# Kernel optimization log

Hardware: AMD Instinct MI355X
Metric: run time of the kernel (lower is better)

## Reference

```python
import jax, jax.numpy as jnp
import numpy as np

V, H, E, L = 50257, 1024, 1024, 512


def setup_inputs() -> dict:
    key = jax.random.key(0)
    ks = jax.random.split(key, 16)
    s = 0.02  # init scale
    return {
        "input_token": jax.random.randint(ks[0], (1,), 0, V),
        "hidden": jax.random.normal(ks[1], (1, 1, H), jnp.float32),
        "encoder_outputs": jax.random.normal(ks[2], (L, H), jnp.float32),
        "embedding": jax.random.normal(ks[3], (V, E), jnp.float32) * s,
        "attn_w": jax.random.normal(ks[4], (L, H + E), jnp.float32) * s,
        "attn_b": jnp.zeros((L,), jnp.float32),
        "comb_w": jax.random.normal(ks[5], (E, H + E), jnp.float32) * s,
        "comb_b": jnp.zeros((E,), jnp.float32),
        "w_ih": jax.random.normal(ks[6], (3 * H, E), jnp.float32) * s,
        "w_hh": jax.random.normal(ks[7], (3 * H, H), jnp.float32) * s,
        "b_ih": jnp.zeros((3 * H,), jnp.float32),
        "b_hh": jnp.zeros((3 * H,), jnp.float32),
        "out_w": jax.random.normal(ks[8], (V, H), jnp.float32) * s,
        "out_b": jnp.zeros((V,), jnp.float32),
    }


def reference(input_token, hidden, encoder_outputs, embedding, attn_w, attn_b,
              comb_w, comb_b, w_ih, w_hh, b_ih, b_hh, out_w, out_b):
    # embedded = embedding(input).view(1,1,-1); dropout is identity in eval
    emb = embedding[input_token].reshape(1, E)            # [1, E]
    h0 = hidden[0]                                        # [1, H]
    # attention over encoder positions
    attn_logits = jnp.concatenate([emb, h0], axis=1) @ attn_w.T + attn_b  # [1, L]
    attn_weights = jax.nn.softmax(attn_logits, axis=1)
    attn_applied = attn_weights @ encoder_outputs         # [1, H]
    # combine + relu
    x = jnp.concatenate([emb, attn_applied], axis=1) @ comb_w.T + comb_b  # [1, E]
    x = jax.nn.relu(x)
    # single GRU cell step (PyTorch gate order: r, z, n)
    gi = x @ w_ih.T + b_ih                                # [1, 3H]
    gh = h0 @ w_hh.T + b_hh                               # [1, 3H]
    i_r, i_z, i_n = jnp.split(gi, 3, axis=1)
    h_r, h_z, h_n = jnp.split(gh, 3, axis=1)
    r = jax.nn.sigmoid(i_r + h_r)
    z = jax.nn.sigmoid(i_z + h_z)
    n = jnp.tanh(i_n + r * h_n)
    h_new = (1.0 - z) * n + z * h0                        # [1, H]
    # output projection + log softmax
    logits = h_new @ out_w.T + out_b                      # [1, V]
    out = jax.nn.log_softmax(logits, axis=1)
    return out, h_new[None], attn_weights
```

## Files before the change

kernel.cpp:

```cpp
#include <hip/hip_runtime.h>

#define V 50257
#define H 1024
#define E 1024
#define LENC 512

__device__ __forceinline__ float wave_reduce_sum(float v) {
    #pragma unroll
    for (int off = 32; off > 0; off >>= 1)
        v += __shfl_down(v, off, 64);
    return v;
}

__global__ void dotcat_kernel(const float* __restrict__ W,
                              const float* __restrict__ bias,
                              const float* __restrict__ emb_table,
                              const int*   __restrict__ token,
                              const float* __restrict__ b,
                              float* __restrict__ out,
                              int relu) {
    int wid = threadIdx.x >> 6, lane = threadIdx.x & 63;
    int row = blockIdx.x * 4 + wid;
    const float4* w4 = (const float4*)(W + (size_t)row * 2048);
    const float4* e4 = (const float4*)(emb_table + (size_t)(*token) * 1024);
    const float4* b4 = (const float4*)b;
    float acc = 0.f;
    #pragma unroll
    for (int j = 0; j < 4; ++j) {
        float4 w = w4[lane + 64 * j];
        float4 x = e4[lane + 64 * j];
        acc += w.x * x.x + w.y * x.y + w.z * x.z + w.w * x.w;
    }
    #pragma unroll
    for (int j = 0; j < 4; ++j) {
        float4 w = w4[256 + lane + 64 * j];
        float4 x = b4[lane + 64 * j];
        acc += w.x * x.x + w.y * x.y + w.z * x.z + w.w * x.w;
    }
    acc = wave_reduce_sum(acc);
    if (lane == 0) {
        acc += bias[row];
        if (relu) acc = fmaxf(acc, 0.0f);
        out[row] = acc;
    }
}

__global__ void softmax512_kernel(const float* __restrict__ in,
                                  float* __restrict__ out,
                                  float* __restrict__ aapp) {
    int t = threadIdx.x;
    aapp[t] = 0.f;
    aapp[512 + t] = 0.f;
    float x = in[t];
    float m = x;
    #pragma unroll
    for (int off = 32; off > 0; off >>= 1)
        m = fmaxf(m, __shfl_down(m, off, 64));
    __shared__ float sm[8];
    __shared__ float ss[8];
    int lane = t & 63, wid = t >> 6;
    if (lane == 0) sm[wid] = m;
    __syncthreads();
    if (t == 0) {
        float mm = sm[0];
        #pragma unroll
        for (int i = 1; i < 8; ++i) mm = fmaxf(mm, sm[i]);
        sm[0] = mm;
    }
    __syncthreads();
    float M = sm[0];
    float e = expf(x - M);
    float s = e;
    #pragma unroll
    for (int off = 32; off > 0; off >>= 1)
        s += __shfl_down(s, off, 64);
    if (lane == 0) ss[wid] = s;
    __syncthreads();
    if (t == 0) {
        float tot = 0.f;
        #pragma unroll
        for (int i = 0; i < 8; ++i) tot += ss[i];
        ss[0] = tot;
    }
    __syncthreads();
    out[t] = e / ss[0];
}

__global__ void attn_apply_kernel(const float* __restrict__ weights,
                                  const float* __restrict__ enc,
                                  float* __restrict__ aapp) {
    int h  = blockIdx.x * 256 + threadIdx.x;
    int l0 = blockIdx.y * 32;
    float acc = 0.f;
    #pragma unroll 8
    for (int l = 0; l < 32; ++l)
        acc += weights[l0 + l] * enc[(size_t)(l0 + l) * 1024 + h];
    atomicAdd(&aapp[h], acc);
}

__global__ void gru_fused_kernel(const float* __restrict__ w_ih,
                                 const float* __restrict__ w_hh,
                                 const float* __restrict__ b_ih,
                                 const float* __restrict__ b_hh,
                                 const float* __restrict__ x,
                                 const float* __restrict__ h0,
                                 float* __restrict__ hnew) {
    int j = blockIdx.x;
    int g = threadIdx.x >> 6, lane = threadIdx.x & 63;
    int sel = g / 3;
    int gate = g % 3;
    int row = gate * 1024 + j;
    const float* Wm  = sel ? w_hh : w_ih;
    const float* vin = sel ? h0 : x;
    const float* bia = sel ? b_hh : b_ih;
    const float4* w4 = (const float4*)(Wm + (size_t)row * 1024);
    const float4* v4 = (const float4*)vin;
    float acc = 0.f;
    #pragma unroll
    for (int jj = 0; jj < 4; ++jj) {
        float4 w = w4[lane + 64 * jj];
        float4 v = v4[lane + 64 * jj];
        acc += w.x * v.x + w.y * v.y + w.z * v.z + w.w * v.w;
    }
    acc = wave_reduce_sum(acc);
    __shared__ float s[6];
    if (lane == 0) s[g] = acc + bia[row];
    __syncthreads();
    if (threadIdx.x == 0) {
        float r = 1.0f / (1.0f + expf(-(s[0] + s[3])));
        float z = 1.0f / (1.0f + expf(-(s[1] + s[4])));
        float n = tanhf(s[2] + r * s[5]);
        hnew[j] = (1.0f - z) * n + z * h0[j];
    }
}

__global__ void logits_kernel(const float* __restrict__ out_w,
                              const float* __restrict__ out_b,
                              const float* __restrict__ h,
                              float* __restrict__ logits,
                              float* __restrict__ part) {
    int wid = threadIdx.x >> 6, lane = threadIdx.x & 63;
    int gw = blockIdx.x * 4 + wid;
    const float4* h4 = (const float4*)h;
    float4 x0 = h4[lane], x1 = h4[lane + 64], x2 = h4[lane + 128], x3 = h4[lane + 192];
    float psum = 0.f;
    for (int row = gw; row < V; row += 8192) {
        const float4* w4 = (const float4*)(out_w + (size_t)row * 1024);
        float4 w0 = w4[lane], w1 = w4[lane + 64], w2 = w4[lane + 128], w3 = w4[lane + 192];
        float acc = w0.x * x0.x + w0.y * x0.y + w0.z * x0.z + w0.w * x0.w
                  + w1.x * x1.x + w1.y * x1.y + w1.z * x1.z + w1.w * x1.w
                  + w2.x * x2.x + w2.y * x2.y + w2.z * x2.z + w2.w * x2.w
                  + w3.x * x3.x + w3.y * x3.y + w3.z * x3.z + w3.w * x3.w;
        acc = wave_reduce_sum(acc);
        if (lane == 0) {
            acc += out_b[row];
            logits[row] = acc;
            psum += expf(acc);
        }
    }
    __shared__ float s[4];
    if (lane == 0) s[wid] = psum;
    __syncthreads();
    if (threadIdx.x == 0) part[blockIdx.x] = s[0] + s[1] + s[2] + s[3];
}

__global__ void logsub_kernel(float* __restrict__ out,
                              const float* __restrict__ part) {
    float v = 0.f;
    #pragma unroll
    for (int i = threadIdx.x; i < 2048; i += 256) v += part[i];
    v = wave_reduce_sum(v);
    __shared__ float s[4];
    int lane = threadIdx.x & 63, wid = threadIdx.x >> 6;
    if (lane == 0) s[wid] = v;
    __syncthreads();
    float lse = logf(s[0] + s[1] + s[2] + s[3]);
    int i = blockIdx.x * 256 + threadIdx.x;
    if (i < V) out[i] -= lse;
}

extern "C" void kernel_launch(void* const* d_in, const int* in_sizes, int n_in,
                              void* d_out, int out_size, void* d_ws, size_t ws_size,
                              hipStream_t stream) {
    const int*   token     = (const int*)d_in[0];
    const float* hidden    = (const float*)d_in[1];
    const float* enc       = (const float*)d_in[2];
    const float* emb_table = (const float*)d_in[3];
    const float* attn_w    = (const float*)d_in[4];
    const float* attn_b    = (const float*)d_in[5];
    const float* comb_w    = (const float*)d_in[6];
    const float* comb_b    = (const float*)d_in[7];
    const float* w_ih      = (const float*)d_in[8];
    const float* w_hh      = (const float*)d_in[9];
    const float* b_ih      = (const float*)d_in[10];
    const float* b_hh      = (const float*)d_in[11];
    const float* out_w     = (const float*)d_in[12];
    const float* out_b     = (const float*)d_in[13];

    float* out       = (float*)d_out;
    float* hnew_out  = out + V;
    float* attnw_out = out + V + H;

    float* wsf  = (float*)d_ws;
    float* alog = wsf;
    float* aapp = alog + 512;
    float* xbuf = aapp + 1024;
    float* part = xbuf + 1024;

    dotcat_kernel<<<LENC / 4, 256, 0, stream>>>(attn_w, attn_b, emb_table, token,
                                                hidden, alog, 0);
    softmax512_kernel<<<1, 512, 0, stream>>>(alog, attnw_out, aapp);
    attn_apply_kernel<<<dim3(4, 16), 256, 0, stream>>>(attnw_out, enc, aapp);
    dotcat_kernel<<<E / 4, 256, 0, stream>>>(comb_w, comb_b, emb_table, token,
                                             aapp, xbuf, 1);
    gru_fused_kernel<<<H, 384, 0, stream>>>(w_ih, w_hh, b_ih, b_hh, xbuf, hidden,
                                            hnew_out);
    logits_kernel<<<2048, 256, 0, stream>>>(out_w, out_b, hnew_out, out, part);
    logsub_kernel<<<(V + 255) / 256, 256, 0, stream>>>(out, part);
}
```

Before: 57.96 us.

## Restructure decoder stages and prefetch output weights into cache during dependent chain

```diff
diff --git a/kernel.cpp b/kernel.cpp
--- a/kernel.cpp
+++ b/kernel.cpp
@@ -4,6 +4,8 @@
 #define H 1024
 #define E 1024
 #define LENC 512
+#define GBLK 1024
+#define GWAVES (GBLK * 4)
 
 __device__ __forceinline__ float wave_reduce_sum(float v) {
     #pragma unroll
@@ -12,18 +14,125 @@
     return v;
 }
 
-__global__ void dotcat_kernel(const float* __restrict__ W,
-                              const float* __restrict__ bias,
+__device__ __forceinline__ void prefetch_chunk(const float* __restrict__ out_w,
+                                               int chunk) {
+    const float4* p = (const float4*)out_w + (size_t)chunk * 4096;
+    float acc = 0.f;
+    #pragma unroll 4
+    for (int i = threadIdx.x; i < 4096; i += 256) {
+        float4 v = p[i];
+        acc += v.x + v.y + v.z + v.w;
+    }
+    asm volatile("" ::"v"(acc));
+}
+
+__global__ void stageA_kernel(const float* __restrict__ attn_w,
+                              const float* __restrict__ attn_b,
+                              const float* __restrict__ w_hh,
+                              const float* __restrict__ b_hh,
                               const float* __restrict__ emb_table,
                               const int*   __restrict__ token,
-                              const float* __restrict__ b,
-                              float* __restrict__ out,
-                              int relu) {
+                              const float* __restrict__ hidden,
+                              const float* __restrict__ out_w,
+                              float* __restrict__ alog,
+                              float* __restrict__ g,
+                              float* __restrict__ aapp) {
+    int bx = blockIdx.x;
     int wid = threadIdx.x >> 6, lane = threadIdx.x & 63;
-    int row = blockIdx.x * 4 + wid;
-    const float4* w4 = (const float4*)(W + (size_t)row * 2048);
+    if (bx < 128) {
+        int row = bx * 4 + wid;
+        const float4* w4 = (const float4*)(attn_w + (size_t)row * 2048);
+        const float4* e4 = (const float4*)(emb_table + (size_t)(*token) * 1024);
+        const float4* h4 = (const float4*)hidden;
+        float acc = 0.f;
+        #pragma unroll
+        for (int j = 0; j < 4; ++j) {
+            float4 w = w4[lane + 64 * j];
+            float4 x = e4[lane + 64 * j];
+            acc += w.x * x.x + w.y * x.y + w.z * x.z + w.w * x.w;
+        }
+        #pragma unroll
+        for (int j = 0; j < 4; ++j) {
+            float4 w = w4[256 + lane + 64 * j];
+            float4 x = h4[lane + 64 * j];
+            acc += w.x * x.x + w.y * x.y + w.z * x.z + w.w * x.w;
+        }
+        acc = wave_reduce_sum(acc);
+        if (lane == 0) alog[row] = acc + attn_b[row];
+    } else if (bx < 896) {
+        int row = (bx - 128) * 4 + wid;
+        const float4* w4 = (const float4*)(w_hh + (size_t)row * 1024);
+        const float4* h4 = (const float4*)hidden;
+        float acc = 0.f;
+        #pragma unroll
+        for (int j = 0; j < 4; ++j) {
+            float4 w = w4[lane + 64 * j];
+            float4 x = h4[lane + 64 * j];
+            acc += w.x * x.x + w.y * x.y + w.z * x.z + w.w * x.w;
+        }
+        acc = wave_reduce_sum(acc);
+        if (lane == 0) g[3072 + row] = acc + b_hh[row];
+    } else if (bx == 896) {
+        int t = threadIdx.x;
+        aapp[t] = 0.f; aapp[256 + t] = 0.f; aapp[512 + t] = 0.f; aapp[768 + t] = 0.f;
+    } else {
+        prefetch_chunk(out_w, bx - 897);
+    }
+}
+
+__global__ void stageC_kernel(const float* __restrict__ alog,
+                              const float* __restrict__ enc,
+                              const float* __restrict__ out_w,
+                              float* __restrict__ aapp,
+                              float* __restrict__ attnw_out) {
+    int bx = blockIdx.x;
+    if (bx >= 256) { prefetch_chunk(out_w, 160 + bx - 256); return; }
+    int t = threadIdx.x;
+    int lane = t & 63, wid = t >> 6;
+    __shared__ float eb[512];
+    __shared__ float sm[4], ssum[4];
+    float a0 = alog[t], a1 = alog[t + 256];
+    float m = fmaxf(a0, a1);
+    #pragma unroll
+    for (int off = 32; off > 0; off >>= 1)
+        m = fmaxf(m, __shfl_down(m, off, 64));
+    if (lane == 0) sm[wid] = m;
+    __syncthreads();
+    float M = fmaxf(fmaxf(sm[0], sm[1]), fmaxf(sm[2], sm[3]));
+    float e0 = expf(a0 - M), e1 = expf(a1 - M);
+    eb[t] = e0; eb[t + 256] = e1;
+    float s = e0 + e1;
+    s = wave_reduce_sum(s);
+    if (lane == 0) ssum[wid] = s;
+    __syncthreads();
+    float S = ssum[0] + ssum[1] + ssum[2] + ssum[3];
+    if (bx == 0) {
+        attnw_out[t] = eb[t] / S;
+        attnw_out[t + 256] = eb[t + 256] / S;
+    }
+    int h  = (bx & 3) * 256 + t;
+    int l0 = (bx >> 2) * 8;
+    float acc = 0.f;
+    #pragma unroll
+    for (int l = 0; l < 8; ++l)
+        acc += eb[l0 + l] * enc[(size_t)(l0 + l) * 1024 + h];
+    atomicAdd(&aapp[h], acc / S);
+}
+
+__global__ void stageD_kernel(const float* __restrict__ comb_w,
+                              const float* __restrict__ comb_b,
+                              const float* __restrict__ emb_table,
+                              const int*   __restrict__ token,
+                              const float* __restrict__ aapp,
+                              const float* __restrict__ out_w,
+                              float* __restrict__ xbuf) {
+    int bx = blockIdx.x;
+    if (bx >= 256) { prefetch_chunk(out_w, 320 + bx - 256); return; }
+    int wid = threadIdx.x >> 6, lane = threadIdx.x & 63;
+    int row = bx * 4 + wid;
+    const float4* w4 = (const float4*)(comb_w + (size_t)row * 2048);
     const float4* e4 = (const float4*)(emb_table + (size_t)(*token) * 1024);
-    const float4* b4 = (const float4*)b;
+    const float4* a4 = (const float4*)aapp;
     float acc = 0.f;
     #pragma unroll
     for (int j = 0; j < 4; ++j) {
@@ -34,117 +143,61 @@
     #pragma unroll
     for (int j = 0; j < 4; ++j) {
         float4 w = w4[256 + lane + 64 * j];
-        float4 x = b4[lane + 64 * j];
+        float4 x = a4[lane + 64 * j];
         acc += w.x * x.x + w.y * x.y + w.z * x.z + w.w * x.w;
     }
     acc = wave_reduce_sum(acc);
-    if (lane == 0) {
-        acc += bias[row];
-        if (relu) acc = fmaxf(acc, 0.0f);
-        out[row] = acc;
-    }
-}
-
-__global__ void softmax512_kernel(const float* __restrict__ in,
-                                  float* __restrict__ out,
-                                  float* __restrict__ aapp) {
+    if (lane == 0) xbuf[row] = fmaxf(acc + comb_b[row], 0.0f);
+}
+
+__global__ void stageE_kernel(const float* __restrict__ w_ih,
+                              const float* __restrict__ b_ih,
+                              const float* __restrict__ xbuf,
+                              const float* __restrict__ out_w,
+                              float* __restrict__ g) {
+    int bx = blockIdx.x;
+    if (bx >= 768) { prefetch_chunk(out_w, 480 + bx - 768); return; }
+    int wid = threadIdx.x >> 6, lane = threadIdx.x & 63;
+    int row = bx * 4 + wid;
+    const float4* w4 = (const float4*)(w_ih + (size_t)row * 1024);
+    const float4* x4 = (const float4*)xbuf;
+    float acc = 0.f;
+    #pragma unroll
+    for (int j = 0; j < 4; ++j) {
+        float4 w = w4[lane + 64 * j];
+        float4 x = x4[lane + 64 * j];
+        acc += w.x * x.x + w.y * x.y + w.z * x.z + w.w * x.w;
+    }
+    acc = wave_reduce_sum(acc);
+    if (lane == 0) g[row] = acc + b_ih[row];
+}
+
+__global__ void logits_kernel(const float* __restrict__ g,
+                              const float* __restrict__ hidden,
+                              const float* __restrict__ out_w,
+                              const float* __restrict__ out_b,
+                              float* __restrict__ logits,
+                              float* __restrict__ part,
+                              float* __restrict__ hnew_out) {
+    __shared__ float4 hsm4[256];
+    float* hs = (float*)hsm4;
     int t = threadIdx.x;
-    aapp[t] = 0.f;
-    aapp[512 + t] = 0.f;
-    float x = in[t];
-    float m = x;
-    #pragma unroll
-    for (int off = 32; off > 0; off >>= 1)
-        m = fmaxf(m, __shfl_down(m, off, 64));
-    __shared__ float sm[8];
-    __shared__ float ss[8];
-    int lane = t & 63, wid = t >> 6;
-    if (lane == 0) sm[wid] = m;
-    __syncthreads();
-    if (t == 0) {
-        float mm = sm[0];
-        #pragma unroll
-        for (int i = 1; i < 8; ++i) mm = fmaxf(mm, sm[i]);
-        sm[0] = mm;
-    }
-    __syncthreads();
-    float M = sm[0];
-    float e = expf(x - M);
-    float s = e;
-    #pragma unroll
-    for (int off = 32; off > 0; off >>= 1)
-        s += __shfl_down(s, off, 64);
-    if (lane == 0) ss[wid] = s;
-    __syncthreads();
-    if (t == 0) {
-        float tot = 0.f;
-        #pragma unroll
-        for (int i = 0; i < 8; ++i) tot += ss[i];
-        ss[0] = tot;
-    }
-    __syncthreads();
-    out[t] = e / ss[0];
-}
-
-__global__ void attn_apply_kernel(const float* __restrict__ weights,
-                                  const float* __restrict__ enc,
-                                  float* __restrict__ aapp) {
-    int h  = blockIdx.x * 256 + threadIdx.x;
-    int l0 = blockIdx.y * 32;
-    float acc = 0.f;
-    #pragma unroll 8
-    for (int l = 0; l < 32; ++l)
-        acc += weights[l0 + l] * enc[(size_t)(l0 + l) * 1024 + h];
-    atomicAdd(&aapp[h], acc);
-}
-
-__global__ void gru_fused_kernel(const float* __restrict__ w_ih,
-                                 const float* __restrict__ w_hh,
-                                 const float* __restrict__ b_ih,
-                                 const float* __restrict__ b_hh,
-                                 const float* __restrict__ x,
-                                 const float* __restrict__ h0,
-                                 float* __restrict__ hnew) {
-    int j = blockIdx.x;
-    int g = threadIdx.x >> 6, lane = threadIdx.x & 63;
-    int sel = g / 3;
-    int gate = g % 3;
-    int row = gate * 1024 + j;
-    const float* Wm  = sel ? w_hh : w_ih;
-    const float* vin = sel ? h0 : x;
-    const float* bia = sel ? b_hh : b_ih;
-    const float4* w4 = (const float4*)(Wm + (size_t)row * 1024);
-    const float4* v4 = (const float4*)vin;
-    float acc = 0.f;
-    #pragma unroll
-    for (int jj = 0; jj < 4; ++jj) {
-        float4 w = w4[lane + 64 * jj];
-        float4 v = v4[lane + 64 * jj];
-        acc += w.x * v.x + w.y * v.y + w.z * v.z + w.w * v.w;
-    }
-    acc = wave_reduce_sum(acc);
-    __shared__ float s[6];
-    if (lane == 0) s[g] = acc + bia[row];
-    __syncthreads();
-    if (threadIdx.x == 0) {
-        float r = 1.0f / (1.0f + expf(-(s[0] + s[3])));
-        float z = 1.0f / (1.0f + expf(-(s[1] + s[4])));
-        float n = tanhf(s[2] + r * s[5]);
-        hnew[j] = (1.0f - z) * n + z * h0[j];
-    }
-}
-
-__global__ void logits_kernel(const float* __restrict__ out_w,
-                              const float* __restrict__ out_b,
-                              const float* __restrict__ h,
-                              float* __restrict__ logits,
-                              float* __restrict__ part) {
-    int wid = threadIdx.x >> 6, lane = threadIdx.x & 63;
-    int gw = blockIdx.x * 4 + wid;
-    const float4* h4 = (const float4*)h;
+    for (int j = t; j < 1024; j += 256) {
+        float i_r = g[j], i_z = g[j + 1024], i_n = g[j + 2048];
+        float h_r = g[3072 + j], h_z = g[4096 + j], h_n = g[5120 + j];
+        float r = 1.0f / (1.0f + expf(-(i_r + h_r)));
+        float z = 1.0f / (1.0f + expf(-(i_z + h_z)));
+        float n = tanhf(i_n + r * h_n);
+        float hv = (1.0f - z) * n + z * hidden[j];
+        hs[j] = hv;
+        if (blockIdx.x == 0) hnew_out[j] = hv;
+    }
+    __syncthreads();
+    int wid = t >> 6, lane = t & 63;
+    const float4* h4 = (const float4*)hsm4;
     float4 x0 = h4[lane], x1 = h4[lane + 64], x2 = h4[lane + 128], x3 = h4[lane + 192];
     float psum = 0.f;
-    for (int row = gw; row < V; row += 8192) {
+    for (int row = blockIdx.x * 4 + wid; row < V; row += GWAVES) {
         const float4* w4 = (const float4*)(out_w + (size_t)row * 1024);
         float4 w0 = w4[lane], w1 = w4[lane + 64], w2 = w4[lane + 128], w3 = w4[lane + 192];
         float acc = w0.x * x0.x + w0.y * x0.y + w0.z * x0.z + w0.w * x0.w
@@ -161,21 +214,20 @@
     __shared__ float s[4];
     if (lane == 0) s[wid] = psum;
     __syncthreads();
-    if (threadIdx.x == 0) part[blockIdx.x] = s[0] + s[1] + s[2] + s[3];
+    if (t == 0) part[blockIdx.x] = s[0] + s[1] + s[2] + s[3];
 }
 
 __global__ void logsub_kernel(float* __restrict__ out,
                               const float* __restrict__ part) {
-    float v = 0.f;
-    #pragma unroll
-    for (int i = threadIdx.x; i < 2048; i += 256) v += part[i];
+    int t = threadIdx.x;
+    int lane = t & 63, wid = t >> 6;
+    float v = part[t] + part[t + 256] + part[t + 512] + part[t + 768];
     v = wave_reduce_sum(v);
     __shared__ float s[4];
-    int lane = threadIdx.x & 63, wid = threadIdx.x >> 6;
     if (lane == 0) s[wid] = v;
     __syncthreads();
     float lse = logf(s[0] + s[1] + s[2] + s[3]);
-    int i = blockIdx.x * 256 + threadIdx.x;
+    int i = blockIdx.x * 256 + t;
     if (i < V) out[i] -= lse;
 }
 
@@ -205,16 +257,16 @@
     float* alog = wsf;
     float* aapp = alog + 512;
     float* xbuf = aapp + 1024;
-    float* part = xbuf + 1024;
-
-    dotcat_kernel<<<LENC / 4, 256, 0, stream>>>(attn_w, attn_b, emb_table, token,
-                                                hidden, alog, 0);
-    softmax512_kernel<<<1, 512, 0, stream>>>(alog, attnw_out, aapp);
-    attn_apply_kernel<<<dim3(4, 16), 256, 0, stream>>>(attnw_out, enc, aapp);
-    dotcat_kernel<<<E / 4, 256, 0, stream>>>(comb_w, comb_b, emb_table, token,
-                                             aapp, xbuf, 1);
-    gru_fused_kernel<<<H, 384, 0, stream>>>(w_ih, w_hh, b_ih, b_hh, xbuf, hidden,
+    float* g    = xbuf + 1024;
+    float* part = g + 6144;
+
+    stageA_kernel<<<1057, 256, 0, stream>>>(attn_w, attn_b, w_hh, b_hh, emb_table,
+                                            token, hidden, out_w, alog, g, aapp);
+    stageC_kernel<<<416, 256, 0, stream>>>(alog, enc, out_w, aapp, attnw_out);
+    stageD_kernel<<<416, 256, 0, stream>>>(comb_w, comb_b, emb_table, token, aapp,
+                                           out_w, xbuf);
+    stageE_kernel<<<864, 256, 0, stream>>>(w_ih, b_ih, xbuf, out_w, g);
+    logits_kernel<<<GBLK, 256, 0, stream>>>(g, hidden, out_w, out_b, out, part,
                                             hnew_out);
-    logits_kernel<<<2048, 256, 0, stream>>>(out_w, out_b, hnew_out, out, part);
     logsub_kernel<<<(V + 255) / 256, 256, 0, stream>>>(out, part);
 }
```

Result: slower. 60.24 us (+3.9%).
